# Optimization experiments

Measured on AMD Instinct MI355X. Metric: run time of the kernel, lower is better.

## Reference

```python
import jax, jax.numpy as jnp
import numpy as np
from jax.ops import segment_sum, segment_max

DIM = 64
NUM_FEAT = 14
EDGE_FEAT = 4
OUT_DIM = 16
NUM_GRAPHS = 512
NEG_SLOPE = 0.01


def _leaky(v):
    return jnp.where(v >= 0, v, NEG_SLOPE * v)


def setup_inputs() -> dict:
    key = jax.random.key(0)
    ks = jax.random.split(key, 24)
    N, E = 20000, 40000
    s = 0.1
    inp = {
        "x": jax.random.normal(ks[0], (N, NUM_FEAT), jnp.float32),
        "edge_attr": jax.random.normal(ks[1], (E, EDGE_FEAT), jnp.float32),
        "edge_index": jax.random.randint(ks[2], (2, E), 0, N, jnp.int64) if jax.config.jax_enable_x64 else jax.random.randint(ks[2], (2, E), 0, N).astype(jnp.int32),
        "batch": jnp.sort(jax.random.randint(ks[3], (N,), 0, NUM_GRAPHS)).astype(jnp.int32),
        # lin0
        "lin0_w": s * jax.random.normal(ks[4], (DIM, NUM_FEAT), jnp.float32),
        "lin0_b": s * jax.random.normal(ks[5], (DIM,), jnp.float32),
        # edge network: Linear(4,dim) -> LeakyReLU -> Linear(dim, dim*dim)
        "net_w1": s * jax.random.normal(ks[6], (DIM, EDGE_FEAT), jnp.float32),
        "net_b1": s * jax.random.normal(ks[7], (DIM,), jnp.float32),
        "net_w2": s * jax.random.normal(ks[8], (DIM * DIM, DIM), jnp.float32),
        "net_b2": s * jax.random.normal(ks[9], (DIM * DIM,), jnp.float32),
        # NNConv root weight + bias
        "root_w": s * jax.random.normal(ks[10], (DIM, DIM), jnp.float32),
        "conv_b": s * jax.random.normal(ks[11], (DIM,), jnp.float32),
        # GRU (torch gate order: r, z, n)
        "gru_w_ih": s * jax.random.normal(ks[12], (3 * DIM, DIM), jnp.float32),
        "gru_w_hh": s * jax.random.normal(ks[13], (3 * DIM, DIM), jnp.float32),
        "gru_b_ih": s * jax.random.normal(ks[14], (3 * DIM,), jnp.float32),
        "gru_b_hh": s * jax.random.normal(ks[15], (3 * DIM,), jnp.float32),
        # Set2Set LSTM (input 2*dim, hidden dim; torch gate order: i, f, g, o)
        "lstm_w_ih": s * jax.random.normal(ks[16], (4 * DIM, 2 * DIM), jnp.float32),
        "lstm_w_hh": s * jax.random.normal(ks[17], (4 * DIM, DIM), jnp.float32),
        "lstm_b_ih": s * jax.random.normal(ks[18], (4 * DIM,), jnp.float32),
        "lstm_b_hh": s * jax.random.normal(ks[19], (4 * DIM,), jnp.float32),
        # lin_out
        "lout_w": s * jax.random.normal(ks[20], (OUT_DIM, 2 * DIM), jnp.float32),
        "lout_b": s * jax.random.normal(ks[21], (OUT_DIM,), jnp.float32),
    }
    return inp


def _forward(x, edge_attr, lin0_w, lin0_b, net_w1, net_b1, net_w2, net_b2,
             root_w, conv_b, gru_w_ih, gru_w_hh, gru_b_ih, gru_b_hh,
             lstm_w_ih, lstm_w_hh, lstm_b_ih, lstm_b_hh, lout_w, lout_b,
             edge_index, batch):
    N = x.shape[0]
    src, tgt = edge_index[0], edge_index[1]

    # per-edge dim x dim weight (shared across the 6 steps; edge_attr is static)
    ew = _leaky(edge_attr @ net_w1.T + net_b1) @ net_w2.T + net_b2  # [E, dim*dim]
    ew = ew.reshape(-1, DIM, DIM)  # [E, in, out]

    deg = segment_sum(jnp.ones_like(tgt, jnp.float32), tgt, num_segments=N)
    inv_deg = 1.0 / jnp.maximum(deg, 1.0)

    out = _leaky(x @ lin0_w.T + lin0_b)  # [N, dim]
    h = out
    for _ in range(6):
        msg = jnp.einsum('ed,edo->eo', out[src], ew)  # gather + per-edge matvec
        agg = segment_sum(msg, tgt, num_segments=N) * inv_deg[:, None]  # scatter-mean
        conv = agg + out @ root_w + conv_b
        m = _leaky(conv)
        # GRU cell (seq len 1)
        gi = m @ gru_w_ih.T + gru_b_ih
        gh = h @ gru_w_hh.T + gru_b_hh
        gi_r, gi_z, gi_n = jnp.split(gi, 3, axis=-1)
        gh_r, gh_z, gh_n = jnp.split(gh, 3, axis=-1)
        r = jax.nn.sigmoid(gi_r + gh_r)
        z = jax.nn.sigmoid(gi_z + gh_z)
        n = jnp.tanh(gi_n + r * gh_n)
        h = (1.0 - z) * n + z * h
        out = h

    # Set2Set, processing_steps=1
    B = NUM_GRAPHS
    q_star = jnp.zeros((B, 2 * DIM), x.dtype)
    h_l = jnp.zeros((B, DIM), x.dtype)
    c_l = jnp.zeros((B, DIM), x.dtype)
    gates = q_star @ lstm_w_ih.T + lstm_b_ih + h_l @ lstm_w_hh.T + lstm_b_hh
    gi_, gf_, gg_, go_ = jnp.split(gates, 4, axis=-1)
    i_g = jax.nn.sigmoid(gi_)
    f_g = jax.nn.sigmoid(gf_)
    g_g = jnp.tanh(gg_)
    o_g = jax.nn.sigmoid(go_)
    c = f_g * c_l + i_g * g_g
    q = o_g * jnp.tanh(c)  # [B, dim]

    e = jnp.sum(out * q[batch], axis=-1)  # [N]
    emax = segment_max(e, batch, num_segments=B)
    emax = jnp.where(jnp.isfinite(emax), emax, 0.0)
    ex = jnp.exp(e - emax[batch])
    denom = segment_sum(ex, batch, num_segments=B)
    a = ex / jnp.maximum(denom, 1e-16)[batch]
    r_read = segment_sum(a[:, None] * out, batch, num_segments=B)  # [B, dim]
    q_star = jnp.concatenate([q, r_read], axis=-1)  # [B, 2*dim]

    return q_star @ lout_w.T + lout_b  # [B, out_dim]


def reference(x, edge_attr, edge_index, batch, lin0_w, lin0_b, net_w1, net_b1,
              net_w2, net_b2, root_w, conv_b, gru_w_ih, gru_w_hh, gru_b_ih,
              gru_b_hh, lstm_w_ih, lstm_w_hh, lstm_b_ih, lstm_b_hh, lout_w, lout_b):
    return _forward(x, edge_attr, lin0_w, lin0_b, net_w1, net_b1, net_w2, net_b2,
                    root_w, conv_b, gru_w_ih, gru_w_hh, gru_b_ih, gru_b_hh,
                    lstm_w_ih, lstm_w_hh, lstm_b_ih, lstm_b_hh, lout_w, lout_b,
                    edge_index, batch)
```

## Files before the change

kernel.cpp:

```cpp
#include <hip/hip_runtime.h>
#include <math.h>

#define DIM 64
#define NFEAT 14
#define EFEAT 4
#define ODIM 16
#define NGRAPH 512
#define NEG 0.01f
#define EBLK 160

typedef _Float16 f16;
typedef _Float16 f16x8 __attribute__((ext_vector_type(8)));
typedef float f32x4 __attribute__((ext_vector_type(4)));

#define MFMA(a,b,c) __builtin_amdgcn_mfma_f32_16x16x32_f16(a,b,c,0,0,0)

__device__ __forceinline__ float leaky(float v){ return v >= 0.f ? v : NEG*v; }
__device__ __forceinline__ float sigm(float v){ return 1.f/(1.f+expf(-v)); }

__global__ void k_pack(const float* __restrict__ src, f16* __restrict__ dst, int NC, int transB){
    int i = blockIdx.x*blockDim.x + threadIdx.x;
    if (i >= NC*64) return;
    int j = i & 7, l = (i >> 3) & 63, s = (i >> 9) & 1, CT = i >> 10;
    int k = ((l >> 4) << 3) + 32*s + j;
    int c = CT*16 + (l & 15);
    float v = transB ? src[(size_t)k*NC + c] : src[(size_t)c*64 + k];
    dst[i] = (f16)v;
}

__global__ void k_hid(const float* __restrict__ ea, const float* __restrict__ w1,
                      const float* __restrict__ b1, f16* __restrict__ hid16, int E){
    int i = blockIdx.x*blockDim.x + threadIdx.x;
    if (i >= E*DIM) return;
    int e = i >> 6, k = i & 63;
    const float* a = ea + (size_t)e*EFEAT;
    const float* w = w1 + k*EFEAT;
    float v = b1[k] + a[0]*w[0] + a[1]*w[1] + a[2]*w[2] + a[3]*w[3];
    hid16[i] = (f16)leaky(v);
}

__global__ void k_deg(const int* __restrict__ ei, float* __restrict__ deg, int E){
    int e = blockIdx.x*blockDim.x + threadIdx.x;
    if (e < E) atomicAdd(&deg[ei[E + e]], 1.0f);
}

__global__ void k_invdeg(float* __restrict__ deg, int N){
    int i = blockIdx.x*blockDim.x + threadIdx.x;
    if (i < N) deg[i] = 1.0f / fmaxf(deg[i], 1.0f);
}

__global__ void k_lin0(const float* __restrict__ x, const float* __restrict__ w,
                       const float* __restrict__ b, float* __restrict__ hf,
                       f16* __restrict__ out16, int N){
    int i = blockIdx.x*blockDim.x + threadIdx.x;
    if (i >= N*DIM) return;
    int n = i >> 6, o = i & 63;
    const float* xr = x + (size_t)n*NFEAT;
    const float* wr = w + o*NFEAT;
    float v = b[o];
#pragma unroll
    for (int f = 0; f < NFEAT; ++f) v += xr[f]*wr[f];
    v = leaky(v);
    hf[i] = v; out16[i] = (f16)v;
}

__global__ __launch_bounds__(256) void k_nbias(const f16x8* __restrict__ out16v,
                                               const f16x8* __restrict__ b2f,
                                               float* __restrict__ nb, int N){
    int n0 = blockIdx.x*64;
    int tid = threadIdx.x, w = tid >> 6, l = tid & 63, li = l & 15, lh = l >> 4;
    int ar = n0 + 16*w + li;
    f16x8 a0{}, a1{};
    if (ar < N){ a0 = out16v[(size_t)ar*8 + lh]; a1 = out16v[(size_t)ar*8 + lh + 4]; }
    f32x4 z = {0.f,0.f,0.f,0.f};
#pragma unroll
    for (int ct = 0; ct < 4; ++ct){
        f32x4 p = MFMA(a0, b2f[(ct*2+0)*64 + l], z);
        p = MFMA(a1, b2f[(ct*2+1)*64 + l], p);
#pragma unroll
        for (int reg = 0; reg < 4; ++reg){
            int n = n0 + 16*w + lh*4 + reg;
            if (n < N) nb[(size_t)n*64 + ct*16 + li] = p[reg];
        }
    }
}

__global__ __launch_bounds__(320) void k_fmsg(const float* __restrict__ hf,
                                              const f16x8* __restrict__ hid16v,
                                              const f16x8* __restrict__ wpf,
                                              const float* __restrict__ nb,
                                              const int* __restrict__ ei,
                                              float* __restrict__ agg, int E){
    __shared__ f16x8 Wch[2][2048];
    __shared__ float OsT[64][164];
    __shared__ int ssrc[EBLK];
    __shared__ int stgt[EBLK];
    int tid = threadIdx.x;
    int e0 = blockIdx.x*EBLK;
    if (tid < EBLK){
        int e = e0 + tid;
        ssrc[tid] = (e < E) ? ei[e] : -1;
        stgt[tid] = (e < E) ? ei[E + e] : -1;
    }
    __syncthreads();
    for (int i = tid; i < EBLK*64; i += 320){
        int r = i >> 6, d = i & 63;
        int s = ssrc[r];
        OsT[d][r] = (s >= 0) ? hf[(size_t)s*64 + d] : 0.f;
    }
    int w = tid >> 6, l = tid & 63, li = l & 15, lh = l >> 4;
    f16x8 a[2][2];
#pragma unroll
    for (int rt = 0; rt < 2; ++rt){
        int e = e0 + w*32 + rt*16 + li;
        if (e < E){
            a[rt][0] = hid16v[(size_t)e*8 + lh];
            a[rt][1] = hid16v[(size_t)e*8 + lh + 4];
        } else { a[rt][0] = f16x8{}; a[rt][1] = f16x8{}; }
    }
    for (int i = tid; i < 2048; i += 320) Wch[0][i] = wpf[i];

    float acc[2][4][4] = {};
    f32x4 z = {0.f,0.f,0.f,0.f};
    __syncthreads();

    for (int c = 0; c < 16; ++c){
        int cb = c & 1;
        f16x8 p0{},p1{},p2{},p3{},p4{},p5{},p6{};
        if (c < 15){
            const f16x8* src = wpf + (size_t)(c+1)*2048;
            p0 = src[tid];
            p1 = src[tid + 320];
            p2 = src[tid + 640];
            p3 = src[tid + 960];
            p4 = src[tid + 1280];
            p5 = src[tid + 1600];
            if (tid < 128) p6 = src[tid + 1920];
        }
#pragma unroll
        for (int dd = 0; dd < 4; ++dd){
            int d = c*4 + dd;
            f16x8 b[4][2];
#pragma unroll
            for (int ct = 0; ct < 4; ++ct){
                b[ct][0] = Wch[cb][(dd*8 + ct*2 + 0)*64 + l];
                b[ct][1] = Wch[cb][(dd*8 + ct*2 + 1)*64 + l];
            }
            float4 osv0 = *(const float4*)&OsT[d][w*32 + lh*4];
            float4 osv1 = *(const float4*)&OsT[d][w*32 + 16 + lh*4];
            float os0[4] = {osv0.x, osv0.y, osv0.z, osv0.w};
            float os1[4] = {osv1.x, osv1.y, osv1.z, osv1.w};
#pragma unroll
            for (int ct = 0; ct < 4; ++ct){
                f32x4 q0 = MFMA(a[0][0], b[ct][0], z);
                q0 = MFMA(a[0][1], b[ct][1], q0);
                f32x4 q1 = MFMA(a[1][0], b[ct][0], z);
                q1 = MFMA(a[1][1], b[ct][1], q1);
#pragma unroll
                for (int reg = 0; reg < 4; ++reg){
                    acc[0][ct][reg] += os0[reg]*q0[reg];
                    acc[1][ct][reg] += os1[reg]*q1[reg];
                }
            }
        }
        if (c < 15){
            __syncthreads();
            int nbuf = cb ^ 1;
            Wch[nbuf][tid]        = p0;
            Wch[nbuf][tid + 320]  = p1;
            Wch[nbuf][tid + 640]  = p2;
            Wch[nbuf][tid + 960]  = p3;
            Wch[nbuf][tid + 1280] = p4;
            Wch[nbuf][tid + 1600] = p5;
            if (tid < 128) Wch[nbuf][tid + 1920] = p6;
            __syncthreads();
        }
    }

#pragma unroll
    for (int rt = 0; rt < 2; ++rt){
#pragma unroll
        for (int reg = 0; reg < 4; ++reg){
            int row = w*32 + rt*16 + lh*4 + reg;
            int t = stgt[row];
            if (t < 0) continue;
            int s = ssrc[row];
#pragma unroll
            for (int ct = 0; ct < 4; ++ct){
                int col = ct*16 + li;
                atomicAdd(&agg[(size_t)t*64 + col], acc[rt][ct][reg] + nb[(size_t)s*64 + col]);
            }
        }
    }
}

__global__ __launch_bounds__(256) void k_node(float* __restrict__ hf,
                                              f16* __restrict__ out16,
                                              const f16x8* __restrict__ out16v,
                                              float* __restrict__ agg,
                                              const float* __restrict__ invdeg,
                                              const float* __restrict__ convb,
                                              const f16x8* __restrict__ wrf,
                                              const f16x8* __restrict__ wihf,
                                              const f16x8* __restrict__ whhf,
                                              const float* __restrict__ bih,
                                              const float* __restrict__ bhh,
                                              const f16x8* __restrict__ b2f,
                                              float* __restrict__ nb, int N){
    __shared__ f16 Ms[64][72];
    int n0 = blockIdx.x*64;
    int tid = threadIdx.x, w = tid >> 6, l = tid & 63, li = l & 15, lh = l >> 4;
    f32x4 z = {0.f,0.f,0.f,0.f};

    int ar = n0 + 16*w + li;
    f16x8 a0{}, a1{};
    if (ar < N){ a0 = out16v[(size_t)ar*8 + lh]; a1 = out16v[(size_t)ar*8 + lh + 4]; }

    int nrow[4]; float invd[4];
#pragma unroll
    for (int reg = 0; reg < 4; ++reg){
        nrow[reg] = n0 + 16*w + lh*4 + reg;
        invd[reg] = (nrow[reg] < N) ? invdeg[nrow[reg]] : 0.f;
    }

#pragma unroll
    for (int ct = 0; ct < 4; ++ct){
        f32x4 p = MFMA(a0, wrf[(ct*2+0)*64 + l], z);
        p = MFMA(a1, wrf[(ct*2+1)*64 + l], p);
        int col = ct*16 + li;
        float cb = convb[col];
#pragma unroll
        for (int reg = 0; reg < 4; ++reg){
            int n = nrow[reg];
            float m = 0.f;
            if (n < N){
                size_t idx = (size_t)n*64 + col;
                m = leaky(p[reg] + agg[idx]*invd[reg] + cb);
                agg[idx] = 0.f;
            }
            Ms[16*w + lh*4 + reg][col] = (f16)m;
        }
    }
    __syncthreads();

    f16x8 am0 = *(const f16x8*)&Ms[16*w + li][lh*8];
    f16x8 am1 = *(const f16x8*)&Ms[16*w + li][lh*8 + 32];

#pragma unroll
    for (int ctq = 0; ctq < 4; ++ctq){
        int col = ctq*16 + li;
        f32x4 pir = MFMA(am0, wihf[((ctq+0)*2+0)*64 + l], z);
        pir = MFMA(am1, wihf[((ctq+0)*2+1)*64 + l], pir);
        f32x4 piz = MFMA(am0, wihf[((ctq+4)*2+0)*64 + l], z);
        piz = MFMA(am1, wihf[((ctq+4)*2+1)*64 + l], piz);
        f32x4 pin = MFMA(am0, wihf[((ctq+8)*2+0)*64 + l], z);
        pin = MFMA(am1, wihf[((ctq+8)*2+1)*64 + l], pin);
        f32x4 phr = MFMA(a0, whhf[((ctq+0)*2+0)*64 + l], z);
        phr = MFMA(a1, whhf[((ctq+0)*2+1)*64 + l], phr);
        f32x4 phz = MFMA(a0, whhf[((ctq+4)*2+0)*64 + l], z);
        phz = MFMA(a1, whhf[((ctq+4)*2+1)*64 + l], phz);
        f32x4 phn = MFMA(a0, whhf[((ctq+8)*2+0)*64 + l], z);
        phn = MFMA(a1, whhf[((ctq+8)*2+1)*64 + l], phn);
        float bir = bih[col], biz = bih[64+col], bin = bih[128+col];
        float bhr = bhh[col], bhz = bhh[64+col], bhn = bhh[128+col];
        __syncthreads();
#pragma unroll
        for (int reg = 0; reg < 4; ++reg){
            int n = nrow[reg];
            float hnew = 0.f;
            if (n < N){
                float hv = hf[(size_t)n*64 + col];
                float r  = sigm(pir[reg] + bir + phr[reg] + bhr);
                float zz = sigm(piz[reg] + biz + phz[reg] + bhz);
                float nn = tanhf(pin[reg] + bin + r*(phn[reg] + bhn));
                hnew = (1.f - zz)*nn + zz*hv;
                hf[(size_t)n*64 + col] = hnew;
                out16[(size_t)n*64 + col] = (f16)hnew;
            }
            Ms[16*w + lh*4 + reg][col] = (f16)hnew;
        }
    }
    __syncthreads();

    f16x8 an0 = *(const f16x8*)&Ms[16*w + li][lh*8];
    f16x8 an1 = *(const f16x8*)&Ms[16*w + li][lh*8 + 32];
#pragma unroll
    for (int ct = 0; ct < 4; ++ct){
        f32x4 p = MFMA(an0, b2f[(ct*2+0)*64 + l], z);
        p = MFMA(an1, b2f[(ct*2+1)*64 + l], p);
#pragma unroll
        for (int reg = 0; reg < 4; ++reg){
            int n = nrow[reg];
            if (n < N) nb[(size_t)n*64 + ct*16 + li] = p[reg];
        }
    }
}

__global__ void k_q(const float* __restrict__ bih, const float* __restrict__ bhh,
                    float* __restrict__ q){
    int j = threadIdx.x;
    if (j >= 64) return;
    float gi = bih[j]       + bhh[j];
    float gg = bih[128+j]   + bhh[128+j];
    float go = bih[192+j]   + bhh[192+j];
    float c = sigm(gi)*tanhf(gg);
    q[j] = sigm(go)*tanhf(c);
}

__device__ __forceinline__ unsigned fkey(float f){
    unsigned u = __float_as_uint(f);
    return (u >> 31) ? ~u : (u | 0x80000000u);
}

__global__ void k_edot(const float* __restrict__ out, const float* __restrict__ q,
                       const int* __restrict__ batch, float* __restrict__ ebuf,
                       unsigned* __restrict__ emaxk, int N){
    int gw = (blockIdx.x*blockDim.x + threadIdx.x) >> 6;
    int d = threadIdx.x & 63;
    if (gw >= N) return;
    float v = out[(size_t)gw*64 + d] * q[d];
#pragma unroll
    for (int s = 32; s; s >>= 1) v += __shfl_xor(v, s, 64);
    if (d == 0){
        ebuf[gw] = v;
        atomicMax(&emaxk[batch[gw]], fkey(v));
    }
}

__global__ void k_ex(float* __restrict__ ebuf, const unsigned* __restrict__ emaxk,
                     const int* __restrict__ batch, float* __restrict__ denom, int N){
    int n = blockIdx.x*blockDim.x + threadIdx.x;
    if (n >= N) return;
    int b = batch[n];
    unsigned k = emaxk[b];
    float em = (k == 0u) ? 0.f
             : ((k >> 31) ? __uint_as_float(k ^ 0x80000000u) : __uint_as_float(~k));
    float ex = expf(ebuf[n] - em);
    ebuf[n] = ex;
    atomicAdd(&denom[b], ex);
}

__global__ void k_rr(const float* __restrict__ out, const float* __restrict__ ebuf,
                     const float* __restrict__ denom, const int* __restrict__ batch,
                     float* __restrict__ rr, int N){
    int gw = (blockIdx.x*blockDim.x + threadIdx.x) >> 6;
    int o = threadIdx.x & 63;
    if (gw >= N) return;
    int b = batch[gw];
    float a = ebuf[gw] / fmaxf(denom[b], 1e-16f);
    atomicAdd(&rr[(size_t)b*64 + o], a * out[(size_t)gw*64 + o]);
}

__global__ void k_out(const float* __restrict__ q, const float* __restrict__ rr,
                      const float* __restrict__ lw, const float* __restrict__ lb,
                      float* __restrict__ dout){
    int i = blockIdx.x*blockDim.x + threadIdx.x;
    if (i >= NGRAPH*ODIM) return;
    int b = i / ODIM, j = i % ODIM;
    const float* w = lw + j*128;
    float acc = lb[j];
#pragma unroll 8
    for (int d = 0; d < 64; ++d) acc += w[d]*q[d];
    const float* rb = rr + (size_t)b*64;
#pragma unroll 8
    for (int d = 0; d < 64; ++d) acc += w[64+d]*rb[d];
    dout[i] = acc;
}

extern "C" void kernel_launch(void* const* d_in, const int* in_sizes, int n_in,
                              void* d_out, int out_size, void* d_ws, size_t ws_size,
                              hipStream_t stream){
    const float* x     = (const float*)d_in[0];
    const float* ea    = (const float*)d_in[1];
    const int*   ei    = (const int*)  d_in[2];
    const int*   batch = (const int*)  d_in[3];
    const float* lin0w = (const float*)d_in[4];
    const float* lin0b = (const float*)d_in[5];
    const float* w1    = (const float*)d_in[6];
    const float* b1    = (const float*)d_in[7];
    const float* w2    = (const float*)d_in[8];
    const float* b2    = (const float*)d_in[9];
    const float* rootw = (const float*)d_in[10];
    const float* convb = (const float*)d_in[11];
    const float* gwih  = (const float*)d_in[12];
    const float* gwhh  = (const float*)d_in[13];
    const float* gbih  = (const float*)d_in[14];
    const float* gbhh  = (const float*)d_in[15];
    const float* lsbih = (const float*)d_in[18];
    const float* lsbhh = (const float*)d_in[19];
    const float* loutw = (const float*)d_in[20];
    const float* loutb = (const float*)d_in[21];

    int N = in_sizes[0] / NFEAT;
    int E = in_sizes[1] / EFEAT;

    char* p = (char*)d_ws;
    size_t off = 0;
    auto carve = [&](size_t bytes) -> void* {
        void* r = p + off;
        off += (bytes + 255) & ~(size_t)255;
        return r;
    };
    f16*      hid16  = (f16*)     carve((size_t)E*64*2);
    float*    hf     = (float*)   carve((size_t)N*64*4);
    f16*      out16  = (f16*)     carve((size_t)N*64*2);
    float*    agg    = (float*)   carve((size_t)N*64*4);
    float*    nb     = (float*)   carve((size_t)N*64*4);
    float*    invdeg = (float*)   carve((size_t)N*4);
    float*    qv     = (float*)   carve(64*4);
    float*    ebuf   = (float*)   carve((size_t)N*4);
    unsigned* emaxk  = (unsigned*)carve(NGRAPH*4);
    float*    denom  = (float*)   carve(NGRAPH*4);
    float*    rr     = (float*)   carve((size_t)NGRAPH*64*4);
    f16*      wpf    = (f16*)     carve((size_t)4096*64*2);
    f16*      wrf    = (f16*)     carve(64*64*2);
    f16*      b2f    = (f16*)     carve(64*64*2);
    f16*      wihf   = (f16*)     carve(192*64*2);
    f16*      whhf   = (f16*)     carve(192*64*2);

    hipMemsetAsync(invdeg, 0, (size_t)N*4, stream);
    hipMemsetAsync(emaxk, 0, NGRAPH*4, stream);
    hipMemsetAsync(denom, 0, NGRAPH*4, stream);
    hipMemsetAsync(rr,    0, (size_t)NGRAPH*64*4, stream);
    hipMemsetAsync(agg,   0, (size_t)N*64*4, stream);

    k_pack<<<(4096*64 + 255)/256, 256, 0, stream>>>(w2,    wpf,  4096, 0);
    k_pack<<<(64*64   + 255)/256, 256, 0, stream>>>(rootw, wrf,  64,   1);
    k_pack<<<(64*64   + 255)/256, 256, 0, stream>>>(b2,    b2f,  64,   1);
    k_pack<<<(192*64  + 255)/256, 256, 0, stream>>>(gwih,  wihf, 192,  0);
    k_pack<<<(192*64  + 255)/256, 256, 0, stream>>>(gwhh,  whhf, 192,  0);

    k_hid<<<((size_t)E*64 + 255)/256, 256, 0, stream>>>(ea, w1, b1, hid16, E);
    k_deg<<<(E + 255)/256, 256, 0, stream>>>(ei, invdeg, E);
    k_invdeg<<<(N + 255)/256, 256, 0, stream>>>(invdeg, N);
    k_lin0<<<((size_t)N*64 + 255)/256, 256, 0, stream>>>(x, lin0w, lin0b, hf, out16, N);

    int eb  = (E + EBLK - 1)/EBLK;
    int nbk = (N + 63)/64;
    int node_grid = ((size_t)N*64 + 255)/256;

    k_nbias<<<nbk, 256, 0, stream>>>((const f16x8*)out16, (const f16x8*)b2f, nb, N);
    for (int it = 0; it < 6; ++it){
        k_fmsg<<<eb, 320, 0, stream>>>(hf, (const f16x8*)hid16, (const f16x8*)wpf,
                                       nb, ei, agg, E);
        k_node<<<nbk, 256, 0, stream>>>(hf, out16, (const f16x8*)out16, agg, invdeg,
                                        convb, (const f16x8*)wrf, (const f16x8*)wihf,
                                        (const f16x8*)whhf, gbih, gbhh,
                                        (const f16x8*)b2f, nb, N);
    }

    k_q<<<1, 64, 0, stream>>>(lsbih, lsbhh, qv);
    k_edot<<<node_grid, 256, 0, stream>>>(hf, qv, batch, ebuf, emaxk, N);
    k_ex<<<(N + 255)/256, 256, 0, stream>>>(ebuf, emaxk, batch, denom, N);
    k_rr<<<node_grid, 256, 0, stream>>>(hf, ebuf, denom, batch, rr, N);
    k_out<<<(NGRAPH*ODIM + 255)/256, 256, 0, stream>>>(qv, rr, loutw, loutb, (float*)d_out);
}
```

Measured before the change: 555.0 us.

## Fold source features into MFMA A operand and split fmsg over input dims

The edge-message kernel now scales the f16 hidden-edge A fragments by the source feature before each MFMA, so the MFMAs accumulate directly instead of producing per-d partial products that are then multiplied and summed in scalar FP32. The input-dimension loop is split across two grid slices (blockIdx.y), each loading half of the packed weights and contributing a partial sum by atomic add. Only slice 0 adds the node-bias term. Source features are stored in f16 in shared memory, and the five workspace memsets are merged into one contiguous memset. The costs are lower precision (f16 product of hidden value and feature), doubled atomics into agg, and repeated loads of the edge A fragments per slice.

Result: slower. 568.1 us (+2.4%).

```diff
diff --git a/kernel.cpp b/kernel.cpp
--- a/kernel.cpp
+++ b/kernel.cpp
@@ -8,6 +8,7 @@
 #define NGRAPH 512
 #define NEG 0.01f
 #define EBLK 160
+#define DSPLIT 2
 
 typedef _Float16 f16;
 typedef _Float16 f16x8 __attribute__((ext_vector_type(8)));
@@ -92,21 +93,23 @@
                                               const int* __restrict__ ei,
                                               float* __restrict__ agg, int E){
     __shared__ f16x8 Wch[2][2048];
-    __shared__ float OsT[64][164];
+    __shared__ f16 OsT[32][168];
     __shared__ int ssrc[EBLK];
     __shared__ int stgt[EBLK];
     int tid = threadIdx.x;
     int e0 = blockIdx.x*EBLK;
+    int dz = blockIdx.y;
+    int dbase = dz*32;
     if (tid < EBLK){
         int e = e0 + tid;
         ssrc[tid] = (e < E) ? ei[e] : -1;
         stgt[tid] = (e < E) ? ei[E + e] : -1;
     }
     __syncthreads();
-    for (int i = tid; i < EBLK*64; i += 320){
-        int r = i >> 6, d = i & 63;
+    for (int i = tid; i < EBLK*32; i += 320){
+        int r = i % EBLK, dl = i / EBLK;
         int s = ssrc[r];
-        OsT[d][r] = (s >= 0) ? hf[(size_t)s*64 + d] : 0.f;
+        OsT[dl][r] = (s >= 0) ? (f16)hf[(size_t)s*64 + dbase + dl] : (f16)0.f;
     }
     int w = tid >> 6, l = tid & 63, li = l & 15, lh = l >> 4;
     f16x8 a[2][2];
@@ -118,17 +121,18 @@
             a[rt][1] = hid16v[(size_t)e*8 + lh + 4];
         } else { a[rt][0] = f16x8{}; a[rt][1] = f16x8{}; }
     }
-    for (int i = tid; i < 2048; i += 320) Wch[0][i] = wpf[i];
-
-    float acc[2][4][4] = {};
-    f32x4 z = {0.f,0.f,0.f,0.f};
+    {
+        const f16x8* wsrc0 = wpf + (size_t)dbase*512;
+        for (int i = tid; i < 2048; i += 320) Wch[0][i] = wsrc0[i];
+    }
+    f32x4 acc[2][4] = {};
     __syncthreads();
 
-    for (int c = 0; c < 16; ++c){
+    for (int c = 0; c < 8; ++c){
         int cb = c & 1;
         f16x8 p0{},p1{},p2{},p3{},p4{},p5{},p6{};
-        if (c < 15){
-            const f16x8* src = wpf + (size_t)(c+1)*2048;
+        if (c < 7){
+            const f16x8* src = wpf + (size_t)(dbase + (c+1)*4)*512;
             p0 = src[tid];
             p1 = src[tid + 320];
             p2 = src[tid + 640];
@@ -139,40 +143,31 @@
         }
 #pragma unroll
         for (int dd = 0; dd < 4; ++dd){
-            int d = c*4 + dd;
-            f16x8 b[4][2];
+            int dl = c*4 + dd;
+            f16 s0 = OsT[dl][w*32 + li];
+            f16 s1 = OsT[dl][w*32 + 16 + li];
+            f16x8 as00 = a[0][0]*s0, as01 = a[0][1]*s0;
+            f16x8 as10 = a[1][0]*s1, as11 = a[1][1]*s1;
 #pragma unroll
             for (int ct = 0; ct < 4; ++ct){
-                b[ct][0] = Wch[cb][(dd*8 + ct*2 + 0)*64 + l];
-                b[ct][1] = Wch[cb][(dd*8 + ct*2 + 1)*64 + l];
+                f16x8 b0 = Wch[cb][(dd*8 + ct*2 + 0)*64 + l];
+                f16x8 b1 = Wch[cb][(dd*8 + ct*2 + 1)*64 + l];
+                acc[0][ct] = MFMA(as00, b0, acc[0][ct]);
+                acc[0][ct] = MFMA(as01, b1, acc[0][ct]);
+                acc[1][ct] = MFMA(as10, b0, acc[1][ct]);
+                acc[1][ct] = MFMA(as11, b1, acc[1][ct]);
             }
-            float4 osv0 = *(const float4*)&OsT[d][w*32 + lh*4];
-            float4 osv1 = *(const float4*)&OsT[d][w*32 + 16 + lh*4];
-            float os0[4] = {osv0.x, osv0.y, osv0.z, osv0.w};
-            float os1[4] = {osv1.x, osv1.y, osv1.z, osv1.w};
-#pragma unroll
-            for (int ct = 0; ct < 4; ++ct){
-                f32x4 q0 = MFMA(a[0][0], b[ct][0], z);
-                q0 = MFMA(a[0][1], b[ct][1], q0);
-                f32x4 q1 = MFMA(a[1][0], b[ct][0], z);
-                q1 = MFMA(a[1][1], b[ct][1], q1);
-#pragma unroll
-                for (int reg = 0; reg < 4; ++reg){
-                    acc[0][ct][reg] += os0[reg]*q0[reg];
-                    acc[1][ct][reg] += os1[reg]*q1[reg];
-                }
-            }
-        }
-        if (c < 15){
+        }
+        if (c < 7){
             __syncthreads();
-            int nbuf = cb ^ 1;
-            Wch[nbuf][tid]        = p0;
-            Wch[nbuf][tid + 320]  = p1;
-            Wch[nbuf][tid + 640]  = p2;
-            Wch[nbuf][tid + 960]  = p3;
-            Wch[nbuf][tid + 1280] = p4;
-            Wch[nbuf][tid + 1600] = p5;
-            if (tid < 128) Wch[nbuf][tid + 1920] = p6;
+            int nb2 = cb ^ 1;
+            Wch[nb2][tid]        = p0;
+            Wch[nb2][tid + 320]  = p1;
+            Wch[nb2][tid + 640]  = p2;
+            Wch[nb2][tid + 960]  = p3;
+            Wch[nb2][tid + 1280] = p4;
+            Wch[nb2][tid + 1600] = p5;
+            if (tid < 128) Wch[nb2][tid + 1920] = p6;
             __syncthreads();
         }
     }
@@ -188,7 +183,9 @@
 #pragma unroll
             for (int ct = 0; ct < 4; ++ct){
                 int col = ct*16 + li;
-                atomicAdd(&agg[(size_t)t*64 + col], acc[rt][ct][reg] + nb[(size_t)s*64 + col]);
+                float v = acc[rt][ct][reg];
+                if (dz == 0) v += nb[(size_t)s*64 + col];
+                atomicAdd(&agg[(size_t)t*64 + col], v);
             }
         }
     }
@@ -404,25 +401,23 @@
     f16*      hid16  = (f16*)     carve((size_t)E*64*2);
     float*    hf     = (float*)   carve((size_t)N*64*4);
     f16*      out16  = (f16*)     carve((size_t)N*64*2);
-    float*    agg    = (float*)   carve((size_t)N*64*4);
     float*    nb     = (float*)   carve((size_t)N*64*4);
-    float*    invdeg = (float*)   carve((size_t)N*4);
     float*    qv     = (float*)   carve(64*4);
     float*    ebuf   = (float*)   carve((size_t)N*4);
-    unsigned* emaxk  = (unsigned*)carve(NGRAPH*4);
-    float*    denom  = (float*)   carve(NGRAPH*4);
-    float*    rr     = (float*)   carve((size_t)NGRAPH*64*4);
     f16*      wpf    = (f16*)     carve((size_t)4096*64*2);
     f16*      wrf    = (f16*)     carve(64*64*2);
     f16*      b2f    = (f16*)     carve(64*64*2);
     f16*      wihf   = (f16*)     carve(192*64*2);
     f16*      whhf   = (f16*)     carve(192*64*2);
-
-    hipMemsetAsync(invdeg, 0, (size_t)N*4, stream);
-    hipMemsetAsync(emaxk, 0, NGRAPH*4, stream);
-    hipMemsetAsync(denom, 0, NGRAPH*4, stream);
-    hipMemsetAsync(rr,    0, (size_t)NGRAPH*64*4, stream);
-    hipMemsetAsync(agg,   0, (size_t)N*64*4, stream);
+    size_t zero_beg = off;
+    float*    agg    = (float*)   carve((size_t)N*64*4);
+    float*    invdeg = (float*)   carve((size_t)N*4);
+    unsigned* emaxk  = (unsigned*)carve(NGRAPH*4);
+    float*    denom  = (float*)   carve(NGRAPH*4);
+    float*    rr     = (float*)   carve((size_t)NGRAPH*64*4);
+    size_t zero_end = off;
+
+    hipMemsetAsync(p + zero_beg, 0, zero_end - zero_beg, stream);
 
     k_pack<<<(4096*64 + 255)/256, 256, 0, stream>>>(w2,    wpf,  4096, 0);
     k_pack<<<(64*64   + 255)/256, 256, 0, stream>>>(rootw, wrf,  64,   1);
@@ -441,8 +436,8 @@
 
     k_nbias<<<nbk, 256, 0, stream>>>((const f16x8*)out16, (const f16x8*)b2f, nb, N);
     for (int it = 0; it < 6; ++it){
-        k_fmsg<<<eb, 320, 0, stream>>>(hf, (const f16x8*)hid16, (const f16x8*)wpf,
-                                       nb, ei, agg, E);
+        k_fmsg<<<dim3(eb, DSPLIT), 320, 0, stream>>>(hf, (const f16x8*)hid16,
+                                                     (const f16x8*)wpf, nb, ei, agg, E);
         k_node<<<nbk, 256, 0, stream>>>(hf, out16, (const f16x8*)out16, agg, invdeg,
                                         convb, (const f16x8*)wrf, (const f16x8*)wihf,
                                         (const f16x8*)whhf, gbih, gbhh,
```
